# Kernel optimization log

Hardware: AMD Instinct MI355X
Metric: run time of the kernel (lower is better)

The kernel has to match this reference:

```python
import jax, jax.numpy as jnp
import numpy as np

# Static module configuration (matches init_kwargs / input_specs)
H, W, C, F = 192, 192, 16, 32
THRES = 0.25
B = 8

def _mask2d(h, w, thres):
    ii, jj = np.meshgrid(np.arange(h), np.arange(w), indexing='ij')
    d = np.sqrt((ii - (h - 1) / 2.0) ** 2 + (jj - (w - 1) / 2.0) ** 2)
    return (d / d.max()) < thres

# Broadcast the spatial low-mode mask over (C, F); tf.where returns row-major
# indices, so flatnonzero of the row-major broadcast mask reproduces the
# exact scatter order of the original layer.
_MASK4 = np.broadcast_to(_mask2d(H, W, THRES)[:, :, None, None], (H, W, C, F))
_FLAT_IDX = np.flatnonzero(np.ascontiguousarray(_MASK4))
N_ACTIVE = int(_FLAT_IDX.size)  # = C * n_modes * F = 1_830_912


def setup_inputs() -> dict:
    key = jax.random.key(0)
    k1, k2, k3 = jax.random.split(key, 3)
    # keras 'random_normal' initializer uses stddev=0.05
    return {
        "inputs": jax.random.normal(k1, (B, H, W, C), dtype=jnp.float32),
        "real_kernel": jax.random.normal(k2, (N_ACTIVE,), dtype=jnp.float32) * 0.05,
        "imag_kernel": jax.random.normal(k3, (N_ACTIVE,), dtype=jnp.float32) * 0.05,
    }


def _scatter_kernel(vals):
    # scatter_nd of the flat weight vector into the (H, W, C, F) grid at the
    # masked (low-frequency) locations, then fftshift over the spatial axes.
    full = jnp.zeros((H * W * C * F,), dtype=vals.dtype).at[_FLAT_IDX].set(vals)
    full = full.reshape(H, W, C, F)
    return jnp.fft.fftshift(full, axes=(0, 1))


def reference(inputs, real_kernel, imag_kernel):
    # fft3d over the last three dims (H, W, C)
    fft_in = jnp.fft.fftn(inputs.astype(jnp.complex64), axes=(1, 2, 3))
    ker = jax.lax.complex(_scatter_kernel(real_kernel), _scatter_kernel(imag_kernel))  # (H,W,C,F) complex64
    # per-frequency (C -> F) mixing: 'abcd,bcde->abce'
    mixed = jnp.einsum('bhwc,hwcf->bhwf', fft_in, ker)
    # ifft3d over (H, W, F), keep the real part
    return jnp.real(jnp.fft.ifftn(mixed, axes=(1, 2, 3))).astype(jnp.float32)
```

## Files before the change

### kernel.cpp

```cpp
#include <hip/hip_runtime.h>
#include <math.h>

#ifndef M_PI
#define M_PI 3.14159265358979323846
#endif

#define HH 192
#define WW 192
#define CC 16
#define FF 32
#define BB 8
#define NBI 68
#define NROW 35
#define NCOL 69
#define ROW0 62
#define MASK_T 4560
#define NWC (WW*CC)
#define SCALE (1.0f/1179648.0f)
#define NDFTH 576

#define OFF_KQ   4096ull
#define OFF_T1   18944000ull
#define OFF_T2   32706560ull
#define OFF_M2   35179520ull
#define OFF_M3   44649472ull
#define T1PART   (BB*NROW*NWC)

__device__ __forceinline__ float2 cmul(float2 a, float2 b) {
    return make_float2(a.x*b.x - a.y*b.y, a.x*b.y + a.y*b.x);
}

__device__ __forceinline__ void build_twiddles(float2* tl, int tid) {
    if (tid < 192) {
        float th = (float)(2.0 * M_PI / 192.0) * (float)tid;
        float s, c;
        sincosf(th, &s, &c);
        tl[tid] = make_float2(c, s);
    }
}

__global__ __launch_bounds__(256) void k_front(
        const float* __restrict__ in, const float* __restrict__ kr,
        const float* __restrict__ ki, float2* __restrict__ KQ,
        float2* __restrict__ T1) {
    int tid = threadIdx.x;
    __shared__ float2 tl[192];
    build_twiddles(tl, tid);
    __syncthreads();

    if (blockIdx.x < NDFTH) {
        int idx = blockIdx.x;
        int b   = idx / 72;
        int rem = idx - b*72;
        int bg  = rem >> 3;
        int zc  = rem & 7;
        int z   = zc >> 1;
        int part = zc & 1;
        int h0 = part * 24;
        const float* inb = in + (size_t)b * HH * NWC;
        int wc0 = z * 768 + tid;
        float2 tw[4], r[4];
        #pragma unroll
        for (int u = 0; u < 4; u++) {
            int row = bg*4 + u;
            int s = row < NROW ? row : 0;
            float2 tv = tl[s];
            r[u] = make_float2(tv.x, -tv.y);
            float2 t0 = tl[(s*h0) % 192];
            tw[u] = make_float2(t0.x, -t0.y);
        }
        float2 acc[4][3];
        #pragma unroll
        for (int u = 0; u < 4; u++)
            #pragma unroll
            for (int k = 0; k < 3; k++) acc[u][k] = make_float2(0.f, 0.f);
        for (int h = h0; h < h0 + 24; h++) {
            const float* p0 = inb + (size_t)h * NWC + wc0;
            const float* p1 = p0 + 48*NWC;
            const float* p2 = p0 + 96*NWC;
            const float* p3 = p0 + 144*NWC;
            float a0=p0[0], a1=p0[256], a2=p0[512];
            float e0=p1[0], e1=p1[256], e2=p1[512];
            float c0=p2[0], c1=p2[256], c2=p2[512];
            float d0=p3[0], d1=p3[256], d2=p3[512];
            float t0_0=a0+c0, t1_0=e0+d0, t2_0=a0-c0, t3_0=e0-d0;
            float t0_1=a1+c1, t1_1=e1+d1, t2_1=a1-c1, t3_1=e1-d1;
            float t0_2=a2+c2, t1_2=e2+d2, t2_2=a2-c2, t3_2=e2-d2;
            float v0_0=t0_0+t1_0, v2_0=t0_0-t1_0;
            float v0_1=t0_1+t1_1, v2_1=t0_1-t1_1;
            float v0_2=t0_2+t1_2, v2_2=t0_2-t1_2;
            acc[0][0].x += v0_0*tw[0].x; acc[0][0].y += v0_0*tw[0].y;
            acc[0][1].x += v0_1*tw[0].x; acc[0][1].y += v0_1*tw[0].y;
            acc[0][2].x += v0_2*tw[0].x; acc[0][2].y += v0_2*tw[0].y;
            tw[0] = cmul(tw[0], r[0]);
            acc[1][0].x += t2_0*tw[1].x + t3_0*tw[1].y; acc[1][0].y += t2_0*tw[1].y - t3_0*tw[1].x;
            acc[1][1].x += t2_1*tw[1].x + t3_1*tw[1].y; acc[1][1].y += t2_1*tw[1].y - t3_1*tw[1].x;
            acc[1][2].x += t2_2*tw[1].x + t3_2*tw[1].y; acc[1][2].y += t2_2*tw[1].y - t3_2*tw[1].x;
            tw[1] = cmul(tw[1], r[1]);
            acc[2][0].x += v2_0*tw[2].x; acc[2][0].y += v2_0*tw[2].y;
            acc[2][1].x += v2_1*tw[2].x; acc[2][1].y += v2_1*tw[2].y;
            acc[2][2].x += v2_2*tw[2].x; acc[2][2].y += v2_2*tw[2].y;
            tw[2] = cmul(tw[2], r[2]);
            acc[3][0].x += t2_0*tw[3].x - t3_0*tw[3].y; acc[3][0].y += t2_0*tw[3].y + t3_0*tw[3].x;
            acc[3][1].x += t2_1*tw[3].x - t3_1*tw[3].y; acc[3][1].y += t2_1*tw[3].y + t3_1*tw[3].x;
            acc[3][2].x += t2_2*tw[3].x - t3_2*tw[3].y; acc[3][2].y += t2_2*tw[3].y + t3_2*tw[3].x;
            tw[3] = cmul(tw[3], r[3]);
        }
        #pragma unroll
        for (int u = 0; u < 4; u++) {
            int row = bg*4 + u;
            if (row < NROW) {
                float2* o = T1 + (size_t)part * T1PART + ((size_t)(b*NROW + row)) * NWC + wc0;
                o[0] = acc[u][0]; o[256] = acc[u][1]; o[512] = acc[u][2];
            }
        }
    } else {
        int blk = blockIdx.x - NDFTH;
        int bi = blk / NBI, bj = blk - bi*NBI;
        float2* KQo = KQ + (size_t)blk * (CC*FF);
        int a = 2*(ROW0+bi) - 191;
        int bc = 2*(ROW0+bj) - 191;
        bool masked = (a*a + bc*bc) <= MASK_T;
        if (!masked) {
            for (int e = tid; e < CC*FF; e += 256) KQo[e] = make_float2(0.f, 0.f);
            return;
        }
        __shared__ float2 Kc[CC][FF+1];
        __shared__ float2 VA[4][4][FF];
        __shared__ float2 Kt[CC][FF+1];
        __shared__ float2 WB[CC][8][4];
        __shared__ int cnts[NBI];
        __shared__ int rank_s;
        if (tid < NBI) {
            int ii = ROW0 + tid;
            int aa = 2*ii - 191;
            int rem = MASK_T - aa*aa;
            int q = (int)sqrtf((float)rem);
            while ((q+1)*(q+1) <= rem) q++;
            while (q > 0 && q*q > rem) q--;
            cnts[tid] = ((191 + q) >> 1) - ((192 - q) >> 1) + 1;
        }
        __syncthreads();
        if (tid == 0) {
            int acc = 0;
            for (int i = 0; i < bi; i++) acc += cnts[i];
            int ii = ROW0 + bi;
            int aa = 2*ii - 191;
            int rem = MASK_T - aa*aa;
            int q = (int)sqrtf((float)rem);
            while ((q+1)*(q+1) <= rem) q++;
            while (q > 0 && q*q > rem) q--;
            rank_s = acc + (ROW0 + bj) - ((192 - q) >> 1);
        }
        __syncthreads();
        size_t base = (size_t)rank_s * (CC*FF);
        for (int e = tid; e < CC*FF; e += 256)
            Kc[e>>5][e&31] = make_float2(kr[base+e], ki[base+e]);
        __syncthreads();
        if (tid < 128) {
            int c0 = tid >> 5, f = tid & 31;
            float2 K0 = Kc[c0][f], K1 = Kc[c0+4][f], K2 = Kc[c0+8][f], K3 = Kc[c0+12][f];
            float Px = K0.x+K2.x, Py = K0.y+K2.y;
            float Mx = K0.x-K2.x, My = K0.y-K2.y;
            float Qx = K1.x+K3.x, Qy = K1.y+K3.y;
            float Nx = K1.x-K3.x, Ny = K1.y-K3.y;
            VA[0][c0][f] = make_float2(Px+Qx, Py+Qy);
            VA[2][c0][f] = make_float2(Px-Qx, Py-Qy);
            VA[1][c0][f] = make_float2(Mx+Ny, My-Nx);
            VA[3][c0][f] = make_float2(Mx-Ny, My+Nx);
        }
        __syncthreads();
        #pragma unroll
        for (int rep = 0; rep < 2; rep++) {
            int idx = tid + rep*256;
            int cp = idx >> 5, f = idx & 31;
            int m = cp & 3;
            float2 acc = make_float2(0.f, 0.f);
            #pragma unroll
            for (int c0 = 0; c0 < 4; c0++) {
                float2 w = tl[(12*c0*cp) % 192];
                float2 v = VA[m][c0][f];
                acc.x += v.x*w.x + v.y*w.y;
                acc.y += v.y*w.x - v.x*w.y;
            }
            Kt[cp][f] = acc;
        }
        __syncthreads();
        if (tid < 128) {
            int cp = tid >> 3, f0 = tid & 7;
            float2 T0 = Kt[cp][f0], T1v = Kt[cp][f0+8], T2 = Kt[cp][f0+16], T3 = Kt[cp][f0+24];
            float Px = T0.x+T2.x, Py = T0.y+T2.y;
            float Mx = T0.x-T2.x, My = T0.y-T2.y;
            float Qx = T1v.x+T3.x, Qy = T1v.y+T3.y;
            float Nx = T1v.x-T3.x, Ny = T1v.y-T3.y;
            WB[cp][f0][0] = make_float2(Px+Qx, Py+Qy);
            WB[cp][f0][2] = make_float2(Px-Qx, Py-Qy);
            WB[cp][f0][1] = make_float2(Mx-Ny, My+Nx);
            WB[cp][f0][3] = make_float2(Mx+Ny, My-Nx);
        }
        __syncthreads();
        #pragma unroll
        for (int rep = 0; rep < 2; rep++) {
            int idx = tid + rep*256;
            int cp = idx >> 5, g = idx & 31;
            int m = g & 3;
            float2 acc = make_float2(0.f, 0.f);
            #pragma unroll
            for (int f0 = 0; f0 < 8; f0++) {
                float2 w = tl[(6*f0*g) % 192];
                float2 v = WB[cp][f0][m];
                acc.x += v.x*w.x - v.y*w.y;
                acc.y += v.x*w.y + v.y*w.x;
            }
            KQo[cp*FF + g] = acc;
        }
    }
}

__global__ __launch_bounds__(256) void k_dft_w(
        const float2* __restrict__ T1, float2* __restrict__ T2) {
    int row = blockIdx.x;
    int b   = blockIdx.y;
    int q   = blockIdx.z;
    const int qbase[4] = {0, 17, 35, 52};
    const int qcnt[4]  = {17, 18, 17, 17};
    int base = qbase[q], cnt = qcnt[q];
    int tid = threadIdx.x;
    __shared__ float2 tl[192];
    __shared__ float2 shp[96][CC];
    __shared__ float2 shm[96][CC];
    build_twiddles(tl, tid);
    const float2* src = T1 + ((size_t)(b*NROW + row)) * NWC;
    for (int e = tid; e < 96*CC; e += 256) {
        float2 a0 = src[e];
        float2 a1 = src[e + T1PART];
        float2 b0 = src[e + 96*CC];
        float2 b1 = src[e + 96*CC + T1PART];
        float Sx = a0.x + a1.x, Sy = a0.y + a1.y;
        float Tx = b0.x + b1.x, Ty = b0.y + b1.y;
        shp[e>>4][e&15] = make_float2(Sx + Tx, Sy + Ty);
        shm[e>>4][e&15] = make_float2(Sx - Tx, Sy - Ty);
    }
    __syncthreads();
    int c = tid >> 4;
    int bjL = tid & 15;
    const float2* shsel = ((base + bjL) & 1) ? &shm[0][0] : &shp[0][0];
    float2 tw[2], r[2], acc[2];
    #pragma unroll
    for (int k = 0; k < 2; k++) {
        int off = bjL + 16*k;
        int col = base + off;
        bool valid = off < cnt;
        int sj = (valid ? col : 34) - 34;
        tw[k] = make_float2(1.f, 0.f);
        acc[k] = make_float2(0.f, 0.f);
        int ts = ((sj % 192) + 192) % 192;
        float2 tv = tl[ts];
        r[k] = make_float2(tv.x, -tv.y);
    }
    for (int w = 0; w < 96; w++) {
        float2 av = shsel[w*CC + c];
        #pragma unroll
        for (int k = 0; k < 2; k++) {
            acc[k].x += av.x*tw[k].x - av.y*tw[k].y;
            acc[k].y += av.x*tw[k].y + av.y*tw[k].x;
            tw[k] = cmul(tw[k], r[k]);
        }
    }
    float2* dst = T2 + ((size_t)((b*NROW + row)*NCOL)) * CC;
    #pragma unroll
    for (int k = 0; k < 2; k++) {
        int off = bjL + 16*k;
        int col = base + off;
        if (off < cnt) dst[col*CC + c] = acc[k];
    }
}

__global__ __launch_bounds__(256) void k_mix(
        const float2* __restrict__ T2, const float2* __restrict__ KQ,
        float2* __restrict__ M2) {
    int site = blockIdx.x;
    int bi = site / NBI, bj = site - bi*NBI;
    int tid = threadIdx.x;
    int b = tid >> 5;
    int g = tid & 31;
    int row, col;
    bool cj;
    if (bi >= 34) { row = bi - 34; col = bj;      cj = false; }
    else          { row = 34 - bi; col = 68 - bj; cj = true;  }
    const float2* x  = T2 + ((size_t)(b*NROW + row) * NCOL + col) * CC;
    const float2* kq = KQ + (size_t)site * (CC*FF);
    float sgn = cj ? -1.f : 1.f;
    float2 acc = make_float2(0.f, 0.f);
    #pragma unroll
    for (int cp = 0; cp < CC; cp++) {
        float2 xv = x[cp];
        xv.y *= sgn;
        float2 kv = kq[cp*FF + g];
        acc.x += xv.x*kv.x - xv.y*kv.y;
        acc.y += xv.x*kv.y + xv.y*kv.x;
    }
    M2[((size_t)b * (NBI*NBI) + site) * FF + g] = acc;
}

__global__ __launch_bounds__(384) void k_idft_w(
        const float2* __restrict__ M2, float2* __restrict__ M3) {
    int bi = blockIdx.x;
    int b  = blockIdx.y;
    int tid = threadIdx.x;
    int gq = tid & 7;
    int ty = tid >> 3;
    int g0 = gq * 4;
    int y  = ty;
    __shared__ float2 tl[192];
    __shared__ __align__(16) float2 m2s[NBI][FF];
    build_twiddles(tl, tid);
    {
        const float4* src = reinterpret_cast<const float4*>(
            M2 + ((size_t)b*(NBI*NBI) + (size_t)bi*NBI) * FF);
        float4* dst = reinterpret_cast<float4*>(&m2s[0][0]);
        for (int e = tid; e < NBI*FF/2; e += 384) dst[e] = src[e];
    }
    __syncthreads();
    float2 tw = tl[(158*y) % 192];
    float2 rr = tl[y];
    float2 zz = make_float2(0.f, 0.f);
    float2 C0[4] = {zz,zz,zz,zz};
    float2 C1[4] = {zz,zz,zz,zz};
    float2 C2[4] = {zz,zz,zz,zz};
    float2 C3[4] = {zz,zz,zz,zz};
#define IW_STEP(ROW, CL) { \
    float4 e0 = *reinterpret_cast<const float4*>(&m2s[ROW][g0]); \
    float4 e1 = *reinterpret_cast<const float4*>(&m2s[ROW][g0+2]); \
    CL[0].x += e0.x*tw.x - e0.y*tw.y;  CL[0].y += e0.x*tw.y + e0.y*tw.x; \
    CL[1].x += e0.z*tw.x - e0.w*tw.y;  CL[1].y += e0.z*tw.y + e0.w*tw.x; \
    CL[2].x += e1.x*tw.x - e1.y*tw.y;  CL[2].y += e1.x*tw.y + e1.y*tw.x; \
    CL[3].x += e1.z*tw.x - e1.w*tw.y;  CL[3].y += e1.z*tw.y + e1.w*tw.x; \
    tw = cmul(tw, rr); }
    for (int bj = 0; bj < NBI; bj += 4) {
        IW_STEP(bj,   C2)
        IW_STEP(bj+1, C3)
        IW_STEP(bj+2, C0)
        IW_STEP(bj+3, C1)
    }
#undef IW_STEP
    float2 R0[4], R1[4], R2[4], R3[4];
    #pragma unroll
    for (int k = 0; k < 4; k++) {
        float2 p = make_float2(C0[k].x + C2[k].x, C0[k].y + C2[k].y);
        float2 q = make_float2(C1[k].x + C3[k].x, C1[k].y + C3[k].y);
        float2 m = make_float2(C0[k].x - C2[k].x, C0[k].y - C2[k].y);
        float2 n = make_float2(C1[k].x - C3[k].x, C1[k].y - C3[k].y);
        R0[k] = make_float2(p.x + q.x, p.y + q.y);
        R2[k] = make_float2(p.x - q.x, p.y - q.y);
        R1[k] = make_float2(m.x - n.y, m.y + n.x);
        R3[k] = make_float2(m.x + n.y, m.y - n.x);
    }
    float2* p0 = M3 + (((size_t)b*HH + y)*NBI + bi)*FF + g0;
    *reinterpret_cast<float4*>(p0)     = make_float4(R0[0].x,R0[0].y,R0[1].x,R0[1].y);
    *reinterpret_cast<float4*>(p0 + 2) = make_float4(R0[2].x,R0[2].y,R0[3].x,R0[3].y);
    float2* p1 = M3 + (((size_t)b*HH + y + 48)*NBI + bi)*FF + g0;
    *reinterpret_cast<float4*>(p1)     = make_float4(R1[0].x,R1[0].y,R1[1].x,R1[1].y);
    *reinterpret_cast<float4*>(p1 + 2) = make_float4(R1[2].x,R1[2].y,R1[3].x,R1[3].y);
    float2* p2 = M3 + (((size_t)b*HH + y + 96)*NBI + bi)*FF + g0;
    *reinterpret_cast<float4*>(p2)     = make_float4(R2[0].x,R2[0].y,R2[1].x,R2[1].y);
    *reinterpret_cast<float4*>(p2 + 2) = make_float4(R2[2].x,R2[2].y,R2[3].x,R2[3].y);
    float2* p3 = M3 + (((size_t)b*HH + y + 144)*NBI + bi)*FF + g0;
    *reinterpret_cast<float4*>(p3)     = make_float4(R3[0].x,R3[0].y,R3[1].x,R3[1].y);
    *reinterpret_cast<float4*>(p3 + 2) = make_float4(R3[2].x,R3[2].y,R3[3].x,R3[3].y);
}

__global__ __launch_bounds__(256) void k_idft_h(
        const float2* __restrict__ M3, float* __restrict__ out) {
    int y = blockIdx.x;
    int b = blockIdx.y;
    int tid = threadIdx.x;
    const float2* m3s = M3 + ((size_t)b*HH + y)*NBI*FF;
    __shared__ float2 tl[192];
    __shared__ __align__(16) float2 comb[NROW][FF];
    build_twiddles(tl, tid);
    for (int e = tid; e < NROW*FF; e += 256) {
        int p = e >> 5, g = e & 31;
        float A, Bv;
        if (p == 0) {
            float2 v = m3s[34*FF + g];
            A = v.x; Bv = 0.f;
        } else if (p == 34) {
            float2 v = m3s[0*FF + g];
            A = v.x; Bv = -v.y;
        } else {
            float2 vp = m3s[(34 + p)*FF + g];
            float2 vm = m3s[(34 - p)*FF + g];
            A = vp.x + vm.x; Bv = vp.y - vm.y;
        }
        comb[p][g] = make_float2(A, Bv);
    }
    __syncthreads();
    int tx = tid >> 3;
    int tg = tid & 7;
    int g0 = tg * 4;
    float2 tw[3], rr[3];
    float ae[3][4], ao[3][4];
    #pragma unroll
    for (int j = 0; j < 3; j++) {
        int x = tx*3 + j;
        tw[j] = make_float2(1.f, 0.f);
        rr[j] = tl[x];
        #pragma unroll
        for (int q = 0; q < 4; q++) { ae[j][q] = 0.f; ao[j][q] = 0.f; }
    }
    for (int p = 0; p < 34; p += 2) {
        float4 f0 = *reinterpret_cast<const float4*>(&comb[p][g0]);
        float4 f1 = *reinterpret_cast<const float4*>(&comb[p][g0+2]);
        #pragma unroll
        for (int j = 0; j < 3; j++) {
            float2 t = tw[j];
            ae[j][0] += f0.x*t.x - f0.y*t.y;
            ae[j][1] += f0.z*t.x - f0.w*t.y;
            ae[j][2] += f1.x*t.x - f1.y*t.y;
            ae[j][3] += f1.z*t.x - f1.w*t.y;
            tw[j] = cmul(t, rr[j]);
        }
        float4 h0 = *reinterpret_cast<const float4*>(&comb[p+1][g0]);
        float4 h1 = *reinterpret_cast<const float4*>(&comb[p+1][g0+2]);
        #pragma unroll
        for (int j = 0; j < 3; j++) {
            float2 t = tw[j];
            ao[j][0] += h0.x*t.x - h0.y*t.y;
            ao[j][1] += h0.z*t.x - h0.w*t.y;
            ao[j][2] += h1.x*t.x - h1.y*t.y;
            ao[j][3] += h1.z*t.x - h1.w*t.y;
            tw[j] = cmul(t, rr[j]);
        }
    }
    {
        float4 f0 = *reinterpret_cast<const float4*>(&comb[34][g0]);
        float4 f1 = *reinterpret_cast<const float4*>(&comb[34][g0+2]);
        #pragma unroll
        for (int j = 0; j < 3; j++) {
            float2 t = tw[j];
            ae[j][0] += f0.x*t.x - f0.y*t.y;
            ae[j][1] += f0.z*t.x - f0.w*t.y;
            ae[j][2] += f1.x*t.x - f1.y*t.y;
            ae[j][3] += f1.z*t.x - f1.w*t.y;
        }
    }
    #pragma unroll
    for (int j = 0; j < 3; j++) {
        int x = tx*3 + j;
        float4 oA, oB;
        oA.x = (ae[j][0]+ao[j][0])*SCALE; oA.y = (ae[j][1]+ao[j][1])*SCALE;
        oA.z = (ae[j][2]+ao[j][2])*SCALE; oA.w = (ae[j][3]+ao[j][3])*SCALE;
        oB.x = (ae[j][0]-ao[j][0])*SCALE; oB.y = (ae[j][1]-ao[j][1])*SCALE;
        oB.z = (ae[j][2]-ao[j][2])*SCALE; oB.w = (ae[j][3]-ao[j][3])*SCALE;
        *reinterpret_cast<float4*>(&out[(((size_t)(b*HH + x)) * WW + y) * FF + g0]) = oA;
        *reinterpret_cast<float4*>(&out[(((size_t)(b*HH + x + 96)) * WW + y) * FF + g0]) = oB;
    }
}

extern "C" void kernel_launch(void* const* d_in, const int* in_sizes, int n_in,
                              void* d_out, int out_size, void* d_ws, size_t ws_size,
                              hipStream_t stream) {
    const float* in = (const float*)d_in[0];
    const float* kr = (const float*)d_in[1];
    const float* ki = (const float*)d_in[2];
    float* out = (float*)d_out;
    char* ws = (char*)d_ws;
    float2* KQ  = (float2*)(ws + OFF_KQ);
    float2* T1  = (float2*)(ws + OFF_T1);
    float2* T2  = (float2*)(ws + OFF_T2);
    float2* M2  = (float2*)(ws + OFF_M2);
    float2* M3  = (float2*)(ws + OFF_M3);

    k_front <<<dim3(NDFTH + NBI*NBI), 256, 0, stream>>>(in, kr, ki, KQ, T1);
    k_dft_w <<<dim3(NROW, BB, 4), 256, 0, stream>>>(T1, T2);
    k_mix   <<<NBI*NBI, 256, 0, stream>>>(T2, KQ, M2);
    k_idft_w<<<dim3(NBI, BB), 384, 0, stream>>>(M2, M3);
    k_idft_h<<<dim3(HH, BB), 256, 0, stream>>>(M3, out);
}
```

Measured before the change: 111.2 us.

## Fuse frequency-mixing into the inverse W-DFT kernel via shared memory

```diff
diff --git a/kernel.cpp b/kernel.cpp
--- a/kernel.cpp
+++ b/kernel.cpp
@@ -22,7 +22,6 @@
 #define OFF_KQ   4096ull
 #define OFF_T1   18944000ull
 #define OFF_T2   32706560ull
-#define OFF_M2   35179520ull
 #define OFF_M3   44649472ull
 #define T1PART   (BB*NROW*NWC)
 
@@ -276,35 +275,9 @@
     }
 }
 
-__global__ __launch_bounds__(256) void k_mix(
+__global__ __launch_bounds__(384) void k_idft_w(
         const float2* __restrict__ T2, const float2* __restrict__ KQ,
-        float2* __restrict__ M2) {
-    int site = blockIdx.x;
-    int bi = site / NBI, bj = site - bi*NBI;
-    int tid = threadIdx.x;
-    int b = tid >> 5;
-    int g = tid & 31;
-    int row, col;
-    bool cj;
-    if (bi >= 34) { row = bi - 34; col = bj;      cj = false; }
-    else          { row = 34 - bi; col = 68 - bj; cj = true;  }
-    const float2* x  = T2 + ((size_t)(b*NROW + row) * NCOL + col) * CC;
-    const float2* kq = KQ + (size_t)site * (CC*FF);
-    float sgn = cj ? -1.f : 1.f;
-    float2 acc = make_float2(0.f, 0.f);
-    #pragma unroll
-    for (int cp = 0; cp < CC; cp++) {
-        float2 xv = x[cp];
-        xv.y *= sgn;
-        float2 kv = kq[cp*FF + g];
-        acc.x += xv.x*kv.x - xv.y*kv.y;
-        acc.y += xv.x*kv.y + xv.y*kv.x;
-    }
-    M2[((size_t)b * (NBI*NBI) + site) * FF + g] = acc;
-}
-
-__global__ __launch_bounds__(384) void k_idft_w(
-        const float2* __restrict__ M2, float2* __restrict__ M3) {
+        float2* __restrict__ M3) {
     int bi = blockIdx.x;
     int b  = blockIdx.y;
     int tid = threadIdx.x;
@@ -313,13 +286,34 @@
     int g0 = gq * 4;
     int y  = ty;
     __shared__ float2 tl[192];
+    __shared__ __align__(16) float2 t2s[NBI][CC];
     __shared__ __align__(16) float2 m2s[NBI][FF];
     build_twiddles(tl, tid);
-    {
-        const float4* src = reinterpret_cast<const float4*>(
-            M2 + ((size_t)b*(NBI*NBI) + (size_t)bi*NBI) * FF);
-        float4* dst = reinterpret_cast<float4*>(&m2s[0][0]);
-        for (int e = tid; e < NBI*FF/2; e += 384) dst[e] = src[e];
+    for (int e = tid; e < NBI*CC; e += 384) {
+        int bj = e >> 4, cp = e & 15;
+        float2 v;
+        if (bi >= 34) {
+            v = T2[((size_t)(b*NROW + (bi-34))*NCOL + bj)*CC + cp];
+        } else {
+            v = T2[((size_t)(b*NROW + (34-bi))*NCOL + (68-bj))*CC + cp];
+            v.y = -v.y;
+        }
+        t2s[bj][cp] = v;
+    }
+    __syncthreads();
+    const float2* kqb = KQ + (size_t)(bi*NBI) * (CC*FF);
+    for (int e = tid; e < NBI*FF; e += 384) {
+        int bj = e >> 5, g = e & 31;
+        const float2* kq = kqb + (size_t)bj*(CC*FF) + g;
+        float2 acc = make_float2(0.f, 0.f);
+        #pragma unroll
+        for (int cp = 0; cp < CC; cp++) {
+            float2 xv = t2s[bj][cp];
+            float2 kv = kq[cp*FF];
+            acc.x += xv.x*kv.x - xv.y*kv.y;
+            acc.y += xv.x*kv.y + xv.y*kv.x;
+        }
+        m2s[bj][g] = acc;
     }
     __syncthreads();
     float2 tw = tl[(158*y) % 192];
@@ -469,12 +463,10 @@
     float2* KQ  = (float2*)(ws + OFF_KQ);
     float2* T1  = (float2*)(ws + OFF_T1);
     float2* T2  = (float2*)(ws + OFF_T2);
-    float2* M2  = (float2*)(ws + OFF_M2);
     float2* M3  = (float2*)(ws + OFF_M3);
 
     k_front <<<dim3(NDFTH + NBI*NBI), 256, 0, stream>>>(in, kr, ki, KQ, T1);
     k_dft_w <<<dim3(NROW, BB, 4), 256, 0, stream>>>(T1, T2);
-    k_mix   <<<NBI*NBI, 256, 0, stream>>>(T2, KQ, M2);
-    k_idft_w<<<dim3(NBI, BB), 384, 0, stream>>>(M2, M3);
+    k_idft_w<<<dim3(NBI, BB), 384, 0, stream>>>(T2, KQ, M3);
     k_idft_h<<<dim3(HH, BB), 256, 0, stream>>>(M3, out);
 }
```

Result: faster. 107.2 us (median of 4 runs) (-3.6%).
